# Kernel tuning notes

Measured on AMD Instinct MI355X. Metric: run time of the kernel, lower is better.

## Reference

```python
import jax, jax.numpy as jnp
import numpy as np

N = 100000      # nodes
E = 1600000     # edges
DIN, DH, DOUT = 128, 256, 40


def setup_inputs() -> dict:
    key = jax.random.key(0)
    ks = jax.random.split(key, 24)

    def w(i, fan_in, fan_out):
        s = 1.0 / np.sqrt(fan_in)
        return jax.random.uniform(ks[i], (fan_in, fan_out), jnp.float32, -s, s)

    def b(i, fan_in, fan_out):
        s = 1.0 / np.sqrt(fan_in)
        return jax.random.uniform(ks[i], (fan_out,), jnp.float32, -s, s)

    return {
        "x": jax.random.normal(ks[0], (N, DIN), jnp.float32),
        "edge_index": jax.random.randint(ks[1], (2, E), 0, N, dtype=jnp.int64),
        # updates_continues: Linear(DIN,DH), Linear(DH,DH), Linear(DH,DOUT)
        "Wc0": w(2, DIN, DH),  "bc0": b(3, DIN, DH),
        "Wc1": w(4, DH, DH),   "bc1": b(5, DH, DH),
        "Wc2": w(6, DH, DOUT), "bc2": b(7, DH, DOUT),
        # updates_exit: Linear(DIN,DOUT) x2, Linear(DH,DOUT) x2
        "We0": w(8, DIN, DOUT),  "be0": b(9, DIN, DOUT),
        "We1": w(10, DIN, DOUT), "be1": b(11, DIN, DOUT),
        "We2": w(12, DH, DOUT),  "be2": b(13, DH, DOUT),
        "We3": w(14, DH, DOUT),  "be3": b(15, DH, DOUT),
    }


def _gcn_agg(h, src, dst):
    """Symmetric-normalized GCN aggregation with self-loops: D^-1/2 (A+I) D^-1/2 h."""
    ones = jnp.ones(src.shape[0], h.dtype)
    deg = jax.ops.segment_sum(ones, dst, num_segments=N) + 1.0  # self-loop
    dinv = jax.lax.rsqrt(deg)
    coef = dinv[src] * dinv[dst]                    # [E]
    msgs = h[src] * coef[:, None]                   # [E, d] gather
    out = jax.ops.segment_sum(msgs, dst, num_segments=N)  # scatter-add
    return out + h * (dinv * dinv)[:, None]         # self-loop term


def reference(x, edge_index, Wc0, bc0, Wc1, bc1, Wc2, bc2,
              We0, be0, We1, be1, We2, be2, We3, be3):
    src, dst = edge_index[0], edge_index[1]
    Wc = [(Wc0, bc0), (Wc1, bc1), (Wc2, bc2)]
    We = [(We0, be0), (We1, be1), (We2, be2), (We3, be3)]

    h = x
    outs = [jax.nn.log_softmax(h @ We[0][0] + We[0][1], axis=1)]
    for i in range(3):
        h = _gcn_agg(h, src, dst)
        outs.append(jax.nn.log_softmax(h @ We[i + 1][0] + We[i + 1][1], axis=1))
        h = h @ Wc[i][0] + Wc[i][1]
        if i < 2:
            h = jax.nn.relu(h)  # dropout is identity in eval mode
    return jnp.stack(outs, axis=1)  # [N, num_layers+1, DOUT]
```

## Files before the change

### kernel.cpp

```cpp
#include <hip/hip_runtime.h>

#define NNODES 100000
#define NEDGES 1600000
#define NBKT 782

typedef __attribute__((ext_vector_type(8))) short bf16x8;
typedef __attribute__((ext_vector_type(4))) float f32x4;
typedef __attribute__((ext_vector_type(2))) float f32x2;

__device__ __forceinline__ float bf2f(unsigned v) {
  union { unsigned u; float f; } x; x.u = v << 16; return x.f;
}
__device__ __forceinline__ unsigned short f2bf(float f) {
  union { float f; unsigned u; } x; x.f = f;
  unsigned r = x.u + 0x7fffu + ((x.u >> 16) & 1u);
  return (unsigned short)(r >> 16);
}
__device__ __forceinline__ f32x2 unpk(unsigned u) {
  union { unsigned q; float f; } lo, hi;
  lo.q = u << 16; hi.q = u & 0xffff0000u;
  f32x2 r; r.x = lo.f; r.y = hi.f; return r;
}
__device__ __forceinline__ unsigned short ldcv(const void* p, int i, int f32) {
  return f32 ? f2bf(((const float*)p)[i]) : ((const unsigned short*)p)[i];
}
__device__ __forceinline__ int detect_i64(const int* __restrict__ ei) {
  int lane = threadIdx.x & 63;
  int hv = ei[2 * lane + 1];
  unsigned long long nz = __ballot(hv != 0);
  return (__popcll(nz) < 4) ? 1 : 0;
}
__device__ __forceinline__ int edge_at(const int* __restrict__ ei, int j, int i64) {
  return i64 ? ei[2 * j] : ei[j];
}

__global__ void k_zero(int* __restrict__ p, int n) {
  int v = blockIdx.x * blockDim.x + threadIdx.x;
  if (v < n) p[v] = 0;
}


__global__ __launch_bounds__(256) void k_bcnt(const int* __restrict__ ei,
                                              int* __restrict__ bcnt,
                                              const unsigned* __restrict__ xw,
                                              int* __restrict__ flags) {
  __shared__ int h[NBKT];
  __shared__ int cF;
  int t = threadIdx.x;
  for (int i = t; i < NBKT; i += 256) h[i] = 0;
  if (blockIdx.x == 0 && t == 0) cF = 0;
  __syncthreads();
  if (blockIdx.x == 0) {
    int hf = 0;
    for (int i = t; i < 2048; i += 256) {
      unsigned lo = xw[i] & 0xffffu;
      unsigned e = (lo >> 7) & 0xffu;
      if (e >= 0xC0u) hf++;
    }
    atomicAdd(&cF, hf);
  }
  int i64 = detect_i64(ei);
  int e0 = blockIdx.x * 4096;
#pragma unroll
  for (int k = 0; k < 16; ++k) {
    int e = e0 + t + k * 256;
    if (e < NEDGES) {
      int d = edge_at(ei, NEDGES + e, i64);
      if ((unsigned)d < NNODES) atomicAdd(&h[d >> 7], 1);
    }
  }
  __syncthreads();
  for (int i = t; i < NBKT; i += 256)
    if (h[i]) atomicAdd(&bcnt[i], h[i]);
  if (blockIdx.x == 0 && t == 0) flags[0] = (cF > 32) ? 1 : 0;
}

__global__ void k_bscan2(const int* __restrict__ bcnt, int* __restrict__ bbase,
                         int* __restrict__ gcur) {
  int l = threadIdx.x;
  int v[13];
  int s = 0;
#pragma unroll
  for (int k = 0; k < 13; ++k) {
    int j = l * 13 + k;
    v[k] = (j < NBKT) ? bcnt[j] : 0;
    s += v[k];
  }
  int x = s;
#pragma unroll
  for (int o = 1; o < 64; o <<= 1) {
    int y = __shfl_up(x, o, 64);
    if (l >= o) x += y;
  }
  int excl = x - s;
#pragma unroll
  for (int k = 0; k < 13; ++k) {
    int j = l * 13 + k;
    if (j < NBKT) { bbase[j] = excl; gcur[j] = excl; }
    excl += v[k];
  }
  if (l == 63) bbase[NBKT] = x;
}

__global__ __launch_bounds__(256) void k_bstage(const int* __restrict__ ei,
                                                int* __restrict__ gcur,
                                                int* __restrict__ stage) {
  __shared__ int h[NBKT];
  __shared__ int base[NBKT];
  int t = threadIdx.x;
  for (int i = t; i < NBKT; i += 256) h[i] = 0;
  __syncthreads();
  int i64 = detect_i64(ei);
  int e0 = blockIdx.x * 4096;
  int bkt[16], lp[16], rec[16];
#pragma unroll
  for (int k = 0; k < 16; ++k) {
    bkt[k] = -1;
    int e = e0 + t + k * 256;
    if (e < NEDGES) {
      int d = edge_at(ei, NEDGES + e, i64);
      if ((unsigned)d < NNODES) {
        int s = edge_at(ei, e, i64);
        if ((unsigned)s >= NNODES) s = NNODES - 1;
        bkt[k] = d >> 7;
        rec[k] = ((d & 127) << 17) | s;
        lp[k] = atomicAdd(&h[bkt[k]], 1);
      }
    }
  }
  __syncthreads();
  for (int i = t; i < NBKT; i += 256)
    base[i] = h[i] ? atomicAdd(&gcur[i], h[i]) : 0;
  __syncthreads();
#pragma unroll
  for (int k = 0; k < 16; ++k)
    if (bkt[k] >= 0) stage[base[bkt[k]] + lp[k]] = rec[k];
}

__global__ __launch_bounds__(256) void k_bplace(const int* __restrict__ stage,
                                                const int* __restrict__ bbase,
                                                int* __restrict__ offs,
                                                float* __restrict__ dinv,
                                                int* __restrict__ csr_src) {
  __shared__ int h[128];
  __shared__ int cur[128];
  int b = blockIdx.x;
  int t = threadIdx.x;
  int n0 = b * 128;
  int NN = NNODES - n0; if (NN > 128) NN = 128;
  int s0 = bbase[b], s1 = bbase[b + 1];
  int cnt = s1 - s0;
  if (t < 128) h[t] = 0;
  __syncthreads();
  for (int i = t; i < cnt; i += 256) {
    int rec = stage[s0 + i];
    atomicAdd(&h[rec >> 17], 1);
  }
  __syncthreads();
  if (t < 64) {
    int a = h[2 * t], c = h[2 * t + 1];
    int s = a + c;
    int x = s;
#pragma unroll
    for (int o = 1; o < 64; o <<= 1) {
      int y = __shfl_up(x, o, 64);
      if (t >= o) x += y;
    }
    int excl = s0 + x - s;
    cur[2 * t] = excl;
    cur[2 * t + 1] = excl + a;
    if (2 * t < NN) {
      offs[n0 + 2 * t] = excl;
      dinv[n0 + 2 * t] = rsqrtf((float)a + 1.0f);
    }
    if (2 * t + 1 < NN) {
      offs[n0 + 2 * t + 1] = excl + a;
      dinv[n0 + 2 * t + 1] = rsqrtf((float)c + 1.0f);
    }
  }
  if (b == NBKT - 1 && t == 0) offs[NNODES] = s1;
  __syncthreads();
  for (int i = t; i < cnt; i += 256) {
    int rec = stage[s0 + i];
    int pos = atomicAdd(&cur[rec >> 17], 1);
    csr_src[pos] = rec & 0x1FFFF;
  }
}

struct CvtP {
  const void* src[7];
  unsigned short* dst[7];
  int n[7];
  const void* W[6];
  unsigned short* WT[6];
};

__global__ void k_cvt(CvtP p, const int* __restrict__ flags,
                      const float* __restrict__ dinv, unsigned short* __restrict__ xs) {
  int a = blockIdx.y;
  int f32 = flags[0];
  if (a < 7) {
    int n = p.n[a];
    const float* sf = (const float*)p.src[a];
    const unsigned short* sb = (const unsigned short*)p.src[a];
    unsigned short* d = p.dst[a];
    for (int i = blockIdx.x * blockDim.x + threadIdx.x; i < n; i += gridDim.x * blockDim.x) {
      if (a == 0) {
        float v = f32 ? sf[i] : bf2f((unsigned)sb[i]);
        d[i] = f32 ? f2bf(v) : sb[i];
        xs[i] = f2bf(v * dinv[i >> 7]);
      } else {
        d[i] = f32 ? f2bf(sf[i]) : sb[i];
      }
    }
  } else {
    int g = blockIdx.x * 256 + threadIdx.x;
    if (g < 32768) {
      int k = g >> 8, c = g & 255;
      p.WT[0][c * 128 + k] = ldcv(p.W[0], g, f32);
    } else if (g < 98304) {
      int l = g - 32768; int k = l >> 8, c = l & 255;
      p.WT[1][c * 256 + k] = ldcv(p.W[1], l, f32);
    } else if (g < 104448) {
      int l = g - 98304; int c = l >> 7, k = l & 127;
      p.WT[2][l] = (c < 40) ? ldcv(p.W[2], k * 40 + c, f32) : (unsigned short)0;
    } else if (g < 110592) {
      int l = g - 104448; int c = l >> 7, k = l & 127;
      p.WT[3][l] = (c < 40) ? ldcv(p.W[3], k * 40 + c, f32) : (unsigned short)0;
    } else if (g < 122880) {
      int l = g - 110592; int c = l >> 8, k = l & 255;
      p.WT[4][l] = (c < 40) ? ldcv(p.W[4], k * 40 + c, f32) : (unsigned short)0;
    } else if (g < 135168) {
      int l = g - 122880; int c = l >> 8, k = l & 255;
      p.WT[5][l] = (c < 40) ? ldcv(p.W[5], k * 40 + c, f32) : (unsigned short)0;
    }
  }
}

__device__ __forceinline__ void accp(f32x2 (&acc)[4], uint4 u, float w) {
  acc[0] += unpk(u.x) * w;
  acc[1] += unpk(u.y) * w;
  acc[2] += unpk(u.z) * w;
  acc[3] += unpk(u.w) * w;
}

template <int D, int EPB>
__global__ __launch_bounds__(256) void k_agg(
    const unsigned short* __restrict__ hin, unsigned short* __restrict__ hout,
    const int* __restrict__ offs, const int* __restrict__ csr_src,
    const float* __restrict__ dinv) {
  constexpr int LPR = D / 8;
  constexpr int R = 64 / LPR;
  constexpr int NB = EPB / R;
  const int lane = threadIdx.x & 63;
  const int g = lane / LPR;
  const int l = lane % LPR;
  const int v = (blockIdx.x * 256 + threadIdx.x) >> 6;
  if (v >= NNODES) return;

  float dv = dinv[v];
  const size_t vbase = (size_t)v * D + l * 8;
  uint4 su = *(const uint4*)(hin + vbase);
  f32x2 acc[4];
#pragma unroll
  for (int k = 0; k < 4; ++k) acc[k] = (f32x2)0.f;
  accp(acc, su, (g == 0) ? 1.f : 0.f);

  int b0 = offs[v];
  int n = offs[v + 1] - b0;
  if (n > 0) {
    int s[NB];
    float wg[NB];
#pragma unroll
    for (int j = 0; j < NB; ++j) {
      int e = j * R + g;
      int ec = (e < n) ? e : (n - 1);
      s[j] = csr_src[b0 + ec];
      wg[j] = (e < n) ? 1.f : 0.f;
    }
    for (int i = 0; i < n; i += EPB) {
      uint4 gu[NB];
#pragma unroll
      for (int j = 0; j < NB; ++j)
        gu[j] = *(const uint4*)(hin + (size_t)s[j] * D + l * 8);
      float wc[NB];
#pragma unroll
      for (int j = 0; j < NB; ++j) wc[j] = wg[j];
      int i2 = i + EPB;
#pragma unroll
      for (int j = 0; j < NB; ++j) {
        int e = i2 + j * R + g;
        int ec = (e < n) ? e : (n - 1);
        s[j] = csr_src[b0 + ec];
        wg[j] = (e < n) ? 1.f : 0.f;
      }
#pragma unroll
      for (int j = 0; j < NB; ++j) accp(acc, gu[j], wc[j]);
    }
  }
  float a8[8];
#pragma unroll
  for (int k = 0; k < 4; ++k) { a8[2 * k] = acc[k].x; a8[2 * k + 1] = acc[k].y; }
#pragma unroll
  for (int k = 0; k < 8; ++k) {
#pragma unroll
    for (int o = LPR; o < 64; o <<= 1) a8[k] += __shfl_xor(a8[k], o, 64);
  }
  if (g == 0) {
    uint4 ov;
    ov.x = (unsigned)f2bf(dv * a8[0]) | ((unsigned)f2bf(dv * a8[1]) << 16);
    ov.y = (unsigned)f2bf(dv * a8[2]) | ((unsigned)f2bf(dv * a8[3]) << 16);
    ov.z = (unsigned)f2bf(dv * a8[4]) | ((unsigned)f2bf(dv * a8[5]) << 16);
    ov.w = (unsigned)f2bf(dv * a8[6]) | ((unsigned)f2bf(dv * a8[7]) << 16);
    *(uint4*)(hout + vbase) = ov;
  }
}

__global__ __launch_bounds__(256) void k_agg40(
    const unsigned short* __restrict__ P, const int* __restrict__ offs,
    const int* __restrict__ csr_src, const float* __restrict__ dinv,
    const unsigned short* __restrict__ bias, float* __restrict__ outp) {
  const int lane = threadIdx.x & 63;
  const int g = lane >> 5, l = lane & 31;
  const bool act = l < 20;
  const int v = (blockIdx.x * 256 + threadIdx.x) >> 6;
  if (v >= NNODES) return;

  float dv = dinv[v];
  f32x2 a = (f32x2)0.f;
  if (act && g == 0) a = unpk(*(const unsigned*)(P + (size_t)v * 40 + l * 2));
  int b0 = offs[v];
  int n = offs[v + 1] - b0;
  if (n > 0) {
    int s[4];
    float wg[4];
#pragma unroll
    for (int j = 0; j < 4; ++j) {
      int e = j * 2 + g;
      int ec = (e < n) ? e : (n - 1);
      s[j] = csr_src[b0 + ec];
      wg[j] = (e < n) ? 1.f : 0.f;
    }
    for (int i = 0; i < n; i += 8) {
      unsigned gu[4];
#pragma unroll
      for (int j = 0; j < 4; ++j)
        gu[j] = act ? *(const unsigned*)(P + (size_t)s[j] * 40 + l * 2) : 0u;
      float wc[4];
#pragma unroll
      for (int j = 0; j < 4; ++j) wc[j] = wg[j];
      int i2 = i + 8;
#pragma unroll
      for (int j = 0; j < 4; ++j) {
        int e = i2 + j * 2 + g;
        int ec = (e < n) ? e : (n - 1);
        s[j] = csr_src[b0 + ec];
        wg[j] = (e < n) ? 1.f : 0.f;
      }
#pragma unroll
      for (int j = 0; j < 4; ++j) a += unpk(gu[j]) * wc[j];
    }
  }
  a.x += __shfl_xor(a.x, 32, 64);
  a.y += __shfl_xor(a.y, 32, 64);
  float a0 = 0.f, a1 = 0.f;
  if (act) {
    a0 = dv * a.x + bf2f((unsigned)bias[l * 2]);
    a1 = dv * a.y + bf2f((unsigned)bias[l * 2 + 1]);
  }
  float m = act ? fmaxf(a0, a1) : -1e30f;
#pragma unroll
  for (int o = 16; o > 0; o >>= 1) m = fmaxf(m, __shfl_xor(m, o, 32));
  float ss = act ? (expf(a0 - m) + expf(a1 - m)) : 0.f;
#pragma unroll
  for (int o = 16; o > 0; o >>= 1) ss += __shfl_xor(ss, o, 32);
  float ls = logf(ss) + m;
  if (act && g == 0) {
    float2 o2;
    o2.x = a0 - ls;
    o2.y = a1 - ls;
    *(float2*)(outp + (size_t)v * 160 + l * 2) = o2;
  }
}

template <int K, bool SCALE>
__device__ __forceinline__ void mlp_body(
    char* smem, int m0, int c0,
    const unsigned short* __restrict__ A, const unsigned short* __restrict__ WT,
    const unsigned short* __restrict__ bias, unsigned short* __restrict__ out,
    const float* __restrict__ dinv) {
  short* As = (short*)smem;
  short* Bs = (short*)(smem + 10240);
  const int t = threadIdx.x;
  const int lane = t & 63, wv = t >> 6;
  const int mw = (wv >> 1) * 64, nw = (wv & 1) * 64;
  const int lr = lane & 15, lq = lane >> 4;

  f32x4 acc[4][4];
#pragma unroll
  for (int i = 0; i < 4; ++i)
#pragma unroll
    for (int j = 0; j < 4; ++j) acc[i][j] = (f32x4)0.f;

  for (int kc = 0; kc < K; kc += 32) {
    __syncthreads();
#pragma unroll
    for (int it = 0; it < 2; ++it) {
      int idx = t + it * 256;
      int row = idx >> 2, seg = idx & 3;
      uint4 u = make_uint4(0, 0, 0, 0);
      int gr = m0 + row;
      if (gr < NNODES) u = *(const uint4*)(A + (size_t)gr * K + kc + seg * 8);
      *(uint4*)&As[row * 40 + seg * 8] = u;
      uint4 v = *(const uint4*)(WT + (size_t)(c0 + row) * K + kc + seg * 8);
      *(uint4*)&Bs[row * 40 + seg * 8] = v;
    }
    __syncthreads();
    bf16x8 af[4], bfr[4];
#pragma unroll
    for (int i = 0; i < 4; ++i)
      af[i] = *(const bf16x8*)&As[(mw + 16 * i + lr) * 40 + lq * 8];
#pragma unroll
    for (int j = 0; j < 4; ++j)
      bfr[j] = *(const bf16x8*)&Bs[(nw + 16 * j + lr) * 40 + lq * 8];
#pragma unroll
    for (int i = 0; i < 4; ++i)
#pragma unroll
      for (int j = 0; j < 4; ++j)
        acc[i][j] = __builtin_amdgcn_mfma_f32_16x16x32_bf16(af[i], bfr[j], acc[i][j], 0, 0, 0);
  }

  float bv[4];
#pragma unroll
  for (int j = 0; j < 4; ++j) bv[j] = bf2f((unsigned)bias[c0 + nw + 16 * j + lr]);
#pragma unroll
  for (int i = 0; i < 4; ++i) {
    int rbase = m0 + mw + 16 * i + lq * 4;
#pragma unroll
    for (int r = 0; r < 4; ++r) {
      int row = rbase + r;
      if (row < NNODES) {
        float s = SCALE ? dinv[row] : 1.f;
#pragma unroll
        for (int j = 0; j < 4; ++j) {
          int col = c0 + nw + 16 * j + lr;
          float v = fmaxf(acc[i][j][r] + bv[j], 0.f) * s;
          out[(size_t)row * 256 + col] = f2bf(v);
        }
      }
    }
  }
}

template <int K, bool SOFTMAX>
__device__ __forceinline__ void exit_body(
    char* smem, int m0,
    const unsigned short* __restrict__ A, const unsigned short* __restrict__ WT,
    const unsigned short* __restrict__ bias, float* __restrict__ outp,
    unsigned short* __restrict__ Pout, const float* __restrict__ dinv) {
  constexpr int KP = K + 8;
  short* As = (short*)smem;
  short* Bs = (short*)(smem + 10240);
  const int t = threadIdx.x;
  const int lane = t & 63, wv = t >> 6;
  const int mw = wv * 32;
  const int lr = lane & 15, lq = lane >> 4;

  for (int idx = t; idx < 48 * (K / 8); idx += 256) {
    int row = idx / (K / 8), seg = idx % (K / 8);
    uint4 w = *(const uint4*)(WT + (size_t)row * K + seg * 8);
    *(uint4*)&Bs[row * KP + seg * 8] = w;
  }

  f32x4 acc[2][3];
#pragma unroll
  for (int i = 0; i < 2; ++i)
#pragma unroll
    for (int j = 0; j < 3; ++j) acc[i][j] = (f32x4)0.f;

  for (int kc = 0; kc < K; kc += 32) {
    __syncthreads();
#pragma unroll
    for (int it = 0; it < 2; ++it) {
      int idx = t + it * 256;
      int row = idx >> 2, seg = idx & 3;
      uint4 u = make_uint4(0, 0, 0, 0);
      int gr = m0 + row;
      if (gr < NNODES) u = *(const uint4*)(A + (size_t)gr * K + kc + seg * 8);
      *(uint4*)&As[row * 40 + seg * 8] = u;
    }
    __syncthreads();
    bf16x8 af[2], bfr[3];
#pragma unroll
    for (int i = 0; i < 2; ++i)
      af[i] = *(const bf16x8*)&As[(mw + 16 * i + lr) * 40 + lq * 8];
#pragma unroll
    for (int j = 0; j < 3; ++j)
      bfr[j] = *(const bf16x8*)&Bs[(16 * j + lr) * KP + kc + lq * 8];
#pragma unroll
    for (int i = 0; i < 2; ++i)
#pragma unroll
      for (int j = 0; j < 3; ++j)
        acc[i][j] = __builtin_amdgcn_mfma_f32_16x16x32_bf16(af[i], bfr[j], acc[i][j], 0, 0, 0);
  }

  if (SOFTMAX) {
    float bv0 = bf2f((unsigned)bias[lr]);
    float bv1 = bf2f((unsigned)bias[16 + lr]);
    float bv2 = (lr < 8) ? bf2f((unsigned)bias[32 + lr]) : 0.f;
#pragma unroll
    for (int i = 0; i < 2; ++i) {
#pragma unroll
      for (int r = 0; r < 4; ++r) {
        int row = m0 + mw + 16 * i + lq * 4 + r;
        float v0 = acc[i][0][r] + bv0;
        float v1 = acc[i][1][r] + bv1;
        float v2 = (lr < 8) ? (acc[i][2][r] + bv2) : -1e30f;
        float m = fmaxf(fmaxf(v0, v1), v2);
#pragma unroll
        for (int o = 8; o > 0; o >>= 1) m = fmaxf(m, __shfl_xor(m, o, 16));
        float ss = expf(v0 - m) + expf(v1 - m) + ((lr < 8) ? expf(v2 - m) : 0.f);
#pragma unroll
        for (int o = 8; o > 0; o >>= 1) ss += __shfl_xor(ss, o, 16);
        float ls = logf(ss) + m;
        if (row < NNODES) {
          outp[(size_t)row * 160 + lr] = v0 - ls;
          outp[(size_t)row * 160 + 16 + lr] = v1 - ls;
          if (lr < 8) outp[(size_t)row * 160 + 32 + lr] = v2 - ls;
        }
      }
    }
  } else {
#pragma unroll
    for (int i = 0; i < 2; ++i) {
#pragma unroll
      for (int r = 0; r < 4; ++r) {
        int row = m0 + mw + 16 * i + lq * 4 + r;
        if (row < NNODES) {
          float s = dinv[row];
          Pout[(size_t)row * 40 + lr] = f2bf(acc[i][0][r] * s);
          Pout[(size_t)row * 40 + 16 + lr] = f2bf(acc[i][1][r] * s);
          if (lr < 8) Pout[(size_t)row * 40 + 32 + lr] = f2bf(acc[i][2][r] * s);
        }
      }
    }
  }
}

template <int K> struct ExitSM { static constexpr int B = 10240 + 48 * (K + 8) * 2; };

__global__ __launch_bounds__(256) void k_exit0(
    const unsigned short* __restrict__ A, const unsigned short* __restrict__ WT,
    const unsigned short* __restrict__ bias, float* __restrict__ outp,
    const float* __restrict__ dinv) {
  __shared__ __align__(16) char smem[ExitSM<128>::B];
  exit_body<128, true>(smem, blockIdx.x * 128, A, WT, bias, outp, nullptr, dinv);
}

__global__ __launch_bounds__(256) void k_exit3(
    const unsigned short* __restrict__ A, const unsigned short* __restrict__ WT,
    unsigned short* __restrict__ Pout, const float* __restrict__ dinv) {
  __shared__ __align__(16) char smem[ExitSM<256>::B];
  exit_body<256, false>(smem, blockIdx.x * 128, A, WT, nullptr, nullptr, Pout, dinv);
}

template <int K, bool MLPSCALE>
__global__ __launch_bounds__(256) void k_exit_mlp(
    const unsigned short* __restrict__ A,
    const unsigned short* __restrict__ WTmlp, const unsigned short* __restrict__ bmlp,
    unsigned short* __restrict__ outmlp,
    const unsigned short* __restrict__ WTex, const unsigned short* __restrict__ bex,
    float* __restrict__ outp, const float* __restrict__ dinv) {
  constexpr int SM = (ExitSM<K>::B > 20480) ? ExitSM<K>::B : 20480;
  __shared__ __align__(16) char smem[SM];
  int bid = blockIdx.x;
  if (bid < 1564) {
    mlp_body<K, MLPSCALE>(smem, (bid >> 1) * 128, (bid & 1) * 128, A, WTmlp, bmlp, outmlp, dinv);
  } else {
    exit_body<K, true>(smem, (bid - 1564) * 128, A, WTex, bex, outp, nullptr, dinv);
  }
}

extern "C" void kernel_launch(void* const* d_in, const int* in_sizes, int n_in,
                              void* d_out, int out_size, void* d_ws, size_t ws_size,
                              hipStream_t stream) {
  const void* x_raw   = d_in[0];
  const int* ei       = (const int*)d_in[1];
  float* out          = (float*)d_out;

  char* ws = (char*)d_ws;
  int*   flags    = (int*)(ws + 0);
  int*   bcnt     = (int*)(ws + 4096);
  int*   gcur     = (int*)(ws + 8192);
  int*   bbase    = (int*)(ws + 12288);
  float* dinv     = (float*)(ws + 524288);
  int*   offs     = (int*)(ws + 1048576);
  int*   csr_src  = (int*)(ws + 2097152);
  int*   stage    = (int*)(ws + 8650752);
  unsigned short* xb = (unsigned short*)(ws + 16777216);
  unsigned short* wb = (unsigned short*)(ws + 45088768);
  unsigned short* hA = (unsigned short*)(ws + 48234496);
  unsigned short* hB = (unsigned short*)(ws + 100663296);
  unsigned short* xs = hB;
  unsigned short* P  = xb;

  unsigned short* bc0 = wb + 32768;
  unsigned short* bc1 = wb + 98560;
  unsigned short* be0 = wb + 103936;
  unsigned short* be1 = wb + 109096;
  unsigned short* be2 = wb + 119376;
  unsigned short* be3 = wb + 129656;
  unsigned short* WTc0  = wb + 131072;
  unsigned short* WTc1  = wb + 163840;
  unsigned short* WT40e0 = wb + 229376;
  unsigned short* WT40e1 = wb + 235520;
  unsigned short* WT40e2 = wb + 241664;
  unsigned short* WT40e3 = wb + 253952;

  dim3 B(256);
  k_zero<<<dim3(4), B, 0, stream>>>(bcnt, NBKT);
  k_bcnt<<<dim3(391), B, 0, stream>>>(ei, bcnt, (const unsigned*)x_raw, flags);
  k_bscan2<<<dim3(1), dim3(64), 0, stream>>>(bcnt, bbase, gcur);
  k_bstage<<<dim3(391), B, 0, stream>>>(ei, gcur, stage);
  k_bplace<<<dim3(NBKT), B, 0, stream>>>(stage, bbase, offs, dinv, csr_src);

  CvtP p;
  const int bsrc[7] = {0, 3, 5, 9, 11, 13, 15};
  unsigned short* bdst[7] = {xb, bc0, bc1, be0, be1, be2, be3};
  const int bn[7] = {NNODES * 128, 256, 256, 40, 40, 40, 40};
  for (int i = 0; i < 7; ++i) { p.src[i] = d_in[bsrc[i]]; p.dst[i] = bdst[i]; p.n[i] = bn[i]; }
  const int wsrc[6] = {2, 4, 8, 10, 12, 14};
  unsigned short* wdst[6] = {WTc0, WTc1, WT40e0, WT40e1, WT40e2, WT40e3};
  for (int i = 0; i < 6; ++i) { p.W[i] = d_in[wsrc[i]]; p.WT[i] = wdst[i]; }
  k_cvt<<<dim3(1024, 8), B, 0, stream>>>(p, flags, dinv, xs);

  k_exit0<<<dim3(782), B, 0, stream>>>(xb, WT40e0, be0, out + 0 * 40, dinv);
  k_agg<128, 16><<<dim3(25000), B, 0, stream>>>(xs, hA, offs, csr_src, dinv);
  k_exit_mlp<128, true><<<dim3(2346), B, 0, stream>>>(hA, WTc0, bc0, hB,
                                                      WT40e1, be1, out + 1 * 40, dinv);
  k_agg<256, 8><<<dim3(25000), B, 0, stream>>>(hB, hA, offs, csr_src, dinv);
  k_exit_mlp<256, false><<<dim3(2346), B, 0, stream>>>(hA, WTc1, bc1, hB,
                                                       WT40e2, be2, out + 2 * 40, dinv);
  k_exit3<<<dim3(782), B, 0, stream>>>(hB, WT40e3, P, dinv);
  k_agg40<<<dim3(25000), B, 0, stream>>>(P, offs, csr_src, dinv, be3, out + 3 * 40);
}
```

Measured before the change: 623.3 us.

## Split GCN aggregation feature dimension into column partitions per block

The aggregation kernel is changed to handle only a D/P column slice of each node's features per wave, so the grid grows by P. Block indices are interleaved so that consecutive blocks (mod 8) cover different column partitions of the same nodes, which is meant to keep gathered rows hot in cache across partitions and to raise the number of edges handled in parallel per wave (R rises as lanes per row shrink). The cost is P times more index loads and more blocks, with the per-wave edge batch fixed at two gathers per lane group.

```diff
diff --git a/kernel.cpp b/kernel.cpp
--- a/kernel.cpp
+++ b/kernel.cpp
@@ -38,7 +38,6 @@
   int v = blockIdx.x * blockDim.x + threadIdx.x;
   if (v < n) p[v] = 0;
 }
-
 
 __global__ __launch_bounds__(256) void k_bcnt(const int* __restrict__ ei,
                                               int* __restrict__ bcnt,
@@ -244,23 +243,30 @@
   acc[3] += unpk(u.w) * w;
 }
 
-template <int D, int EPB>
-__global__ __launch_bounds__(256) void k_agg(
+template <int D, int P>
+__global__ __launch_bounds__(256) void k_aggp(
     const unsigned short* __restrict__ hin, unsigned short* __restrict__ hout,
     const int* __restrict__ offs, const int* __restrict__ csr_src,
     const float* __restrict__ dinv) {
-  constexpr int LPR = D / 8;
+  constexpr int DP = D / P;
+  constexpr int LPR = DP / 8;
   constexpr int R = 64 / LPR;
-  constexpr int NB = EPB / R;
+  constexpr int NB = 2;
+  constexpr int EPB = NB * R;
+  const int b = blockIdx.x;
+  const int x = b & 7;
+  const int part = x % P;
+  const int nodeblk = (b >> 3) * (8 / P) + x / P;
   const int lane = threadIdx.x & 63;
+  const int wvi = threadIdx.x >> 6;
   const int g = lane / LPR;
   const int l = lane % LPR;
-  const int v = (blockIdx.x * 256 + threadIdx.x) >> 6;
+  const int v = nodeblk * 4 + wvi;
   if (v >= NNODES) return;
 
+  const size_t cbase = (size_t)part * DP + l * 8;
   float dv = dinv[v];
-  const size_t vbase = (size_t)v * D + l * 8;
-  uint4 su = *(const uint4*)(hin + vbase);
+  uint4 su = *(const uint4*)(hin + (size_t)v * D + cbase);
   f32x2 acc[4];
 #pragma unroll
   for (int k = 0; k < 4; ++k) acc[k] = (f32x2)0.f;
@@ -274,15 +280,14 @@
 #pragma unroll
     for (int j = 0; j < NB; ++j) {
       int e = j * R + g;
-      int ec = (e < n) ? e : (n - 1);
-      s[j] = csr_src[b0 + ec];
+      s[j] = csr_src[b0 + (e < n ? e : n - 1)];
       wg[j] = (e < n) ? 1.f : 0.f;
     }
     for (int i = 0; i < n; i += EPB) {
       uint4 gu[NB];
 #pragma unroll
       for (int j = 0; j < NB; ++j)
-        gu[j] = *(const uint4*)(hin + (size_t)s[j] * D + l * 8);
+        gu[j] = *(const uint4*)(hin + (size_t)s[j] * D + cbase);
       float wc[NB];
 #pragma unroll
       for (int j = 0; j < NB; ++j) wc[j] = wg[j];
@@ -290,8 +295,7 @@
 #pragma unroll
       for (int j = 0; j < NB; ++j) {
         int e = i2 + j * R + g;
-        int ec = (e < n) ? e : (n - 1);
-        s[j] = csr_src[b0 + ec];
+        s[j] = csr_src[b0 + (e < n ? e : n - 1)];
         wg[j] = (e < n) ? 1.f : 0.f;
       }
 #pragma unroll
@@ -312,7 +316,7 @@
     ov.y = (unsigned)f2bf(dv * a8[2]) | ((unsigned)f2bf(dv * a8[3]) << 16);
     ov.z = (unsigned)f2bf(dv * a8[4]) | ((unsigned)f2bf(dv * a8[5]) << 16);
     ov.w = (unsigned)f2bf(dv * a8[6]) | ((unsigned)f2bf(dv * a8[7]) << 16);
-    *(uint4*)(hout + vbase) = ov;
+    *(uint4*)(hout + (size_t)v * D + cbase) = ov;
   }
 }
 
@@ -635,10 +639,10 @@
   k_cvt<<<dim3(1024, 8), B, 0, stream>>>(p, flags, dinv, xs);
 
   k_exit0<<<dim3(782), B, 0, stream>>>(xb, WT40e0, be0, out + 0 * 40, dinv);
-  k_agg<128, 16><<<dim3(25000), B, 0, stream>>>(xs, hA, offs, csr_src, dinv);
+  k_aggp<128, 2><<<dim3(50000), B, 0, stream>>>(xs, hA, offs, csr_src, dinv);
   k_exit_mlp<128, true><<<dim3(2346), B, 0, stream>>>(hA, WTc0, bc0, hB,
                                                       WT40e1, be1, out + 1 * 40, dinv);
-  k_agg<256, 8><<<dim3(25000), B, 0, stream>>>(hB, hA, offs, csr_src, dinv);
+  k_aggp<256, 4><<<dim3(100000), B, 0, stream>>>(hB, hA, offs, csr_src, dinv);
   k_exit_mlp<256, false><<<dim3(2346), B, 0, stream>>>(hA, WTc1, bc1, hB,
                                                        WT40e2, be2, out + 2 * 40, dinv);
   k_exit3<<<dim3(782), B, 0, stream>>>(hB, WT40e3, P, dinv);
```

Result: slower. 644.9 us (+3.5%).
